# Kernel optimization log

Hardware: AMD Instinct MI355X
Metric: run time of the kernel (lower is better)

The kernel has to match this reference:

```python
import jax, jax.numpy as jnp
import numpy as np

B, T, S, H, C, E, V, OOV = 8, 16, 400, 512, 512, 128, 50000, 50


def setup_inputs() -> dict:
    key = jax.random.key(0)
    ks = jax.random.split(key, 24)
    rn = lambda k, shape, s=0.05: jax.random.normal(k, shape, dtype=jnp.float32) * s
    inp = {
        'input_embeddings': rn(ks[0], (B, T, E), 1.0),
        'context': rn(ks[1], (B, 1, C), 1.0),
        'h0': rn(ks[2], (1, B, H), 1.0),
        'c0': rn(ks[3], (1, B, H), 1.0),
        'encoder_outputs': rn(ks[4], (B, S, C), 1.0),
        'encoder_masks': jnp.ones((B, S), jnp.float32),
        'extra_zeros': jnp.zeros((B, OOV), jnp.float32),
        'extended_source_idx': jax.random.randint(ks[5], (B, S), 0, V + OOV),
        'coverage': jnp.zeros((B, 1, S), jnp.float32),
        # LSTM (single layer), torch gate order i,f,g,o
        'W_ih': rn(ks[6], (4 * H, E)), 'W_hh': rn(ks[7], (4 * H, H)),
        'b_ih': rn(ks[8], (4 * H,)), 'b_hh': rn(ks[9], (4 * H,)),
        # attention (concat + coverage)
        'cov_w': rn(ks[10], (H, 1)),
        'energy_w': rn(ks[11], (H, H + C)), 'energy_b': rn(ks[12], (H,)),
        'v': jax.random.uniform(ks[13], (H,), jnp.float32),
        # projections
        'xctx_w': rn(ks[14], (E, E + C)), 'xctx_b': rn(ks[15], (E,)),
        'attnd_w': rn(ks[16], (H, H + C)), 'attnd_b': rn(ks[17], (H,)),
        'vocab_w': rn(ks[18], (V, H)), 'vocab_b': rn(ks[19], (V,)),
        'pgen_w': rn(ks[20], (1, C + H + E)), 'pgen_b': rn(ks[21], (1,)),
    }
    return inp


def reference(input_embeddings, context, h0, c0, encoder_outputs, encoder_masks,
              extra_zeros, extended_source_idx, coverage,
              W_ih, W_hh, b_ih, b_hh, cov_w, energy_w, energy_b, v,
              xctx_w, xctx_b, attnd_w, attnd_b, vocab_w, vocab_b, pgen_w, pgen_b):
    Bn = input_embeddings.shape[0]
    Sn = encoder_outputs.shape[1]
    bidx = jnp.arange(Bn)[:, None]

    def step(carry, emb_t):
        h, c, ctx, cov = carry  # [B,H],[B,H],[B,C],[B,S]
        x = jnp.concatenate([emb_t, ctx], -1) @ xctx_w.T + xctx_b  # [B,E]
        gates = x @ W_ih.T + b_ih + h @ W_hh.T + b_hh
        i, f, g, o = jnp.split(gates, 4, axis=-1)
        c_new = jax.nn.sigmoid(f) * c + jax.nn.sigmoid(i) * jnp.tanh(g)
        h_new = jax.nn.sigmoid(o) * jnp.tanh(c_new)  # [B,H]
        # concat-style Luong attention with coverage
        cov_proj = cov[..., None] * cov_w[:, 0]  # [B,S,H] (Linear(1,H) no bias)
        cat = jnp.concatenate([
            jnp.broadcast_to(h_new[:, None, :], (Bn, Sn, h_new.shape[-1])),
            encoder_outputs], -1)  # [B,S,H+C]
        energy = jnp.tanh(cat @ energy_w.T + energy_b + cov_proj)
        e = energy @ v  # [B,S]
        probs = jax.nn.softmax(e, -1) * encoder_masks
        probs = probs / (probs.sum(-1, keepdims=True) + 1e-12)
        ctx_new = jnp.einsum('bs,bsc->bc', probs, encoder_outputs)
        cov_new = cov + probs
        vocab_dist = jax.nn.softmax(
            (jnp.concatenate([h_new, ctx_new], -1) @ attnd_w.T + attnd_b) @ vocab_w.T + vocab_b, -1)
        p_gen = jax.nn.sigmoid(jnp.concatenate([ctx_new, h_new, x], -1) @ pgen_w.T + pgen_b)  # [B,1]
        ext = jnp.concatenate([vocab_dist * p_gen, extra_zeros], 1)  # [B,V+OOV]
        final = ext.at[bidx, extended_source_idx].add((1.0 - p_gen) * probs)
        return (h_new, c_new, ctx_new, cov_new), (final, probs, cov_new, p_gen)

    init = (h0[0], c0[0], context[:, 0], coverage[:, 0])
    (h, c, ctx, cov), (finals, attns, covs, pgens) = jax.lax.scan(
        step, init, jnp.swapaxes(input_embeddings, 0, 1))
    final_vocab_dists = jnp.swapaxes(finals, 0, 1)  # [B,T,V+OOV]
    attn_dists = jnp.swapaxes(attns, 0, 1)          # [B,T,S]
    coverages = jnp.swapaxes(covs, 0, 1)            # [B,T,S]
    return (final_vocab_dists, ctx[:, None, :], h[None], c[None], attn_dists, pgens[-1], coverages)
```

## Files before the change

kernel.cpp:

```cpp
#include <hip/hip_runtime.h>
#include <math.h>

#define BB 8
#define TT 16
#define SS 400
#define HH 512
#define EE 128
#define VV 50000
#define VE 50050
#define OOVn 50

#define O1 6406400
#define O2 6410496
#define O3 6414592
#define O4 6418688
#define O5 6469888
#define O6 6469896

#define G_OFF    0
#define EWHB_OFF 1179648
#define AWBF_OFF 1310720
#define ENCP_OFF 4600000
#define PM_OFF   5700000
#define CTXR_OFF 5800000

typedef __attribute__((ext_vector_type(4))) float floatx4;
typedef __attribute__((ext_vector_type(8))) short short8;
typedef __attribute__((ext_vector_type(8))) unsigned short ushort8_t;
typedef __attribute__((ext_vector_type(4))) unsigned short ushort4_t;

__device__ __forceinline__ float sigm(float x){ return 1.0f/(1.0f+__expf(-x)); }
__device__ __forceinline__ float ftanh(float x){
  float e = __expf(2.0f*x); return 1.0f - 2.0f/(e + 1.0f);
}
__device__ __forceinline__ unsigned short f2bf(float f){
  union { float f; unsigned int u; } v; v.f = f;
  unsigned int u = v.u;
  return (unsigned short)((u + 0x7FFFu + ((u >> 16) & 1u)) >> 16);
}
__device__ __forceinline__ float bfu(unsigned short u){
  union { unsigned int i; float f; } v; v.i = ((unsigned int)u) << 16; return v.f;
}
__device__ __forceinline__ float mac8(const unsigned short* w, const float* u) {
  ushort8_t w8 = *(const ushort8_t*)w;
  float4 u0 = *(const float4*)u;
  float4 u1 = *(const float4*)(u+4);
  return bfu(w8[0])*u0.x + bfu(w8[1])*u0.y + bfu(w8[2])*u0.z + bfu(w8[3])*u0.w
       + bfu(w8[4])*u1.x + bfu(w8[5])*u1.y + bfu(w8[6])*u1.z + bfu(w8[7])*u1.w;
}

__global__ __launch_bounds__(256)
void gemm_bt(const float* __restrict__ A, int lda,
             const float* __restrict__ Bm, int ldb,
             const float* __restrict__ bias,
             float* __restrict__ Cm, int ldc,
             int N, int K, int permute, int obf,
             long bsB, long bsC)
{
  __shared__ unsigned short Ash[128*72];
  __shared__ unsigned short Bsh[64*72];
  int tid = threadIdx.x;
  int mbase = blockIdx.x * 128;
  int nbase = blockIdx.y * 64;
  long z = blockIdx.z;
  const float* Bz = Bm + z*bsB;
  int wave = tid >> 6, lane = tid & 63;
  int wm = (wave & 1) * 64, wn = (wave >> 1) * 32;
  int fl = lane & 15, quad = lane >> 4;

  floatx4 acc[4][2];
  for (int i=0;i<4;i++) for(int j=0;j<2;j++) acc[i][j] = (floatx4)(0.0f);

  for (int kc = 0; kc < K; kc += 64) {
    float4 ra[8], rb[4];
#pragma unroll
    for (int i = 0; i < 8; ++i) {
      int idx = tid + i*256;
      int row = idx >> 4;
      int c4 = (idx & 15) << 2;
      ra[i] = *(const float4*)(A + (size_t)(mbase+row)*lda + kc + c4);
    }
#pragma unroll
    for (int i = 0; i < 4; ++i) {
      int idx = tid + i*256;
      int row = idx >> 4;
      int c4 = (idx & 15) << 2;
      int gn = nbase + row;
      if (gn < N) rb[i] = *(const float4*)(Bz + (size_t)gn*ldb + kc + c4);
      else { rb[i].x = 0.f; rb[i].y = 0.f; rb[i].z = 0.f; rb[i].w = 0.f; }
    }
    __syncthreads();
#pragma unroll
    for (int i = 0; i < 8; ++i) {
      int idx = tid + i*256;
      int o = (idx >> 4)*72 + ((idx & 15) << 2);
      Ash[o+0]=f2bf(ra[i].x); Ash[o+1]=f2bf(ra[i].y); Ash[o+2]=f2bf(ra[i].z); Ash[o+3]=f2bf(ra[i].w);
    }
#pragma unroll
    for (int i = 0; i < 4; ++i) {
      int idx = tid + i*256;
      int o = (idx >> 4)*72 + ((idx & 15) << 2);
      Bsh[o+0]=f2bf(rb[i].x); Bsh[o+1]=f2bf(rb[i].y); Bsh[o+2]=f2bf(rb[i].z); Bsh[o+3]=f2bf(rb[i].w);
    }
    __syncthreads();
#pragma unroll
    for (int ks = 0; ks < 2; ++ks) {
      short8 af[4], bfr[2];
      int ko = ks*32 + quad*8;
#pragma unroll
      for (int i=0;i<4;i++) af[i]  = *(const short8*)&Ash[(wm + i*16 + fl)*72 + ko];
#pragma unroll
      for (int j=0;j<2;j++) bfr[j] = *(const short8*)&Bsh[(wn + j*16 + fl)*72 + ko];
#pragma unroll
      for (int i=0;i<4;i++)
#pragma unroll
        for (int j=0;j<2;j++)
          acc[i][j] = __builtin_amdgcn_mfma_f32_16x16x32_bf16(af[i], bfr[j], acc[i][j], 0,0,0);
    }
    __syncthreads();
  }
  for (int i=0;i<4;i++){
    for (int j=0;j<2;j++){
      int nc = nbase + wn + j*16 + fl;
      if (nc >= N) continue;
      float bv = bias ? bias[nc] : 0.0f;
      for (int r=0;r<4;r++){
        int mg = mbase + wm + i*16 + quad*4 + r;
        int orow = permute ? ((mg & 7)*16 + (mg >> 3)) : mg;
        float v = acc[i][j][r] + bv;
        long ci = (long)orow*ldc + nc + z*bsC;
        if (obf) ((unsigned short*)Cm)[ci] = f2bf(v);
        else     Cm[ci] = v;
      }
    }
  }
}

__global__ __launch_bounds__(256)
void gemm_logits(const unsigned short* __restrict__ Abf,
                 const float* __restrict__ Bm, const float* __restrict__ bias,
                 float* __restrict__ out, float* __restrict__ rowsum)
{
  __shared__ unsigned short Ash[128*72];
  __shared__ unsigned short Bsh[64*72];
  __shared__ float rowpart[128];
  int tid = threadIdx.x;
  int nbase = blockIdx.x * 64;
  int wave = tid >> 6, lane = tid & 63;
  int wm = (wave & 1) * 64, wn = (wave >> 1) * 32;
  int fl = lane & 15, quad = lane >> 4;

  floatx4 acc[4][2];
  for (int i=0;i<4;i++) for(int j=0;j<2;j++) acc[i][j] = (floatx4)(0.0f);
  if (tid < 128) rowpart[tid] = 0.f;

  for (int kc = 0; kc < 512; kc += 64) {
    ushort8_t raa[4];
    float4 rb[4];
#pragma unroll
    for (int i = 0; i < 4; ++i) {
      int idx = tid + i*256;
      int row = idx >> 3;
      int c8 = (idx & 7) << 3;
      raa[i] = *(const ushort8_t*)(Abf + (size_t)row*512 + kc + c8);
    }
#pragma unroll
    for (int i = 0; i < 4; ++i) {
      int idx = tid + i*256;
      int row = idx >> 4;
      int c4 = (idx & 15) << 2;
      int gn = nbase + row;
      if (gn < VV) rb[i] = *(const float4*)(Bm + (size_t)gn*512 + kc + c4);
      else { rb[i].x = 0.f; rb[i].y = 0.f; rb[i].z = 0.f; rb[i].w = 0.f; }
    }
    __syncthreads();
#pragma unroll
    for (int i = 0; i < 4; ++i) {
      int idx = tid + i*256;
      int o = (idx >> 3)*72 + ((idx & 7) << 3);
      *(ushort8_t*)&Ash[o] = raa[i];
    }
#pragma unroll
    for (int i = 0; i < 4; ++i) {
      int idx = tid + i*256;
      int o = (idx >> 4)*72 + ((idx & 15) << 2);
      Bsh[o+0]=f2bf(rb[i].x); Bsh[o+1]=f2bf(rb[i].y); Bsh[o+2]=f2bf(rb[i].z); Bsh[o+3]=f2bf(rb[i].w);
    }
    __syncthreads();
#pragma unroll
    for (int ks = 0; ks < 2; ++ks) {
      short8 af[4], bfr[2];
      int ko = ks*32 + quad*8;
#pragma unroll
      for (int i=0;i<4;i++) af[i]  = *(const short8*)&Ash[(wm + i*16 + fl)*72 + ko];
#pragma unroll
      for (int j=0;j<2;j++) bfr[j] = *(const short8*)&Bsh[(wn + j*16 + fl)*72 + ko];
#pragma unroll
      for (int i=0;i<4;i++)
#pragma unroll
        for (int j=0;j<2;j++)
          acc[i][j] = __builtin_amdgcn_mfma_f32_16x16x32_bf16(af[i], bfr[j], acc[i][j], 0,0,0);
    }
    __syncthreads();
  }
  for (int i=0;i<4;i++){
    for (int r=0;r<4;r++){
      int mg = wm + i*16 + quad*4 + r;
      int orow = (mg & 7)*16 + (mg >> 3);
      float rs = 0.f;
      for (int j=0;j<2;j++){
        int nc = nbase + wn + j*16 + fl;
        if (nc < VV) {
          float e = __expf(acc[i][j][r] + bias[nc]);
          out[(size_t)orow*VE + nc] = e;
          rs += e;
        }
      }
      atomicAdd(&rowpart[mg], rs);
    }
  }
  __syncthreads();
  if (tid < 128) {
    int orow = (tid & 7)*16 + (tid >> 3);
    atomicAdd(&rowsum[orow], rowpart[tid]);
  }
}

__global__ __launch_bounds__(256) void vk_attnd(
    const float* __restrict__ A1, const unsigned short* __restrict__ awbf,
    const float* __restrict__ ab, unsigned short* __restrict__ attnd_bf)
{
  __shared__ float hl[8][1032];
  __shared__ float part[256];
  int tid = threadIdx.x;
  int pc = blockIdx.x & 63;
  int mg = blockIdx.x >> 6;
  int m0 = mg*8;
#pragma unroll
  for (int i = 0; i < 8; ++i)
    *(float4*)&hl[i][tid*4] = *(const float4*)(A1 + (size_t)(m0+i)*1024 + tid*4);
  __syncthreads();
  int dot = tid >> 2, kq = tid & 3;
  int lp = dot >> 3, lm = dot & 7;
  int p = pc*8 + lp;
  const unsigned short* wp = awbf + (size_t)p*1024 + kq*16;
  const float* hh = &hl[lm][kq*16];
  float acc = 0.f;
#pragma unroll
  for (int i = 0; i < 16; ++i) {
    acc += mac8(wp + i*64, hh + i*64);
    acc += mac8(wp + i*64 + 8, hh + i*64 + 8);
  }
  part[tid] = acc;
  __syncthreads();
  if (tid < 64) {
    int lp2 = tid >> 3, lm2 = tid & 7;
    int p2 = pc*8 + lp2;
    float v = ab[p2] + part[tid*4] + part[tid*4+1] + part[tid*4+2] + part[tid*4+3];
    attnd_bf[(size_t)(m0+lm2)*512 + p2] = f2bf(v);
  }
}

__global__ __launch_bounds__(256) void p_wx(const float* __restrict__ wih,
    const float* __restrict__ whh, const float* __restrict__ xcw,
    unsigned short* __restrict__ G)
{
  int blk = blockIdx.x, tid = threadIdx.x;
  if (blk < 640) {
    int rt = blk / 10, ct = blk % 10;
    __shared__ float wl[32*128];
    __shared__ float xl[128*64];
    for (int i = tid; i < 4096; i += 256) {
      int r = i >> 7, k = i & 127;
      wl[i] = wih[(size_t)(rt*32+r)*128 + k];
    }
    for (int i = tid; i < 8192; i += 256) {
      int e = i >> 6, c = i & 63;
      xl[i] = xcw[(size_t)e*640 + ct*64 + c];
    }
    __syncthreads();
    for (int o = tid; o < 2048; o += 256) {
      int r = o >> 6, c = o & 63;
      float acc = 0.f;
      for (int e = 0; e < 128; ++e) acc += wl[r*128+e]*xl[e*64+c];
      G[(size_t)(rt*32+r)*1152 + ct*64 + c] = f2bf(acc);
    }
  } else {
    int idx = blk - 640;
    for (int q = 0; q < 2; ++q) {
      int n = idx*2048 + q*1024 + tid*4;
      int r = n >> 9, k = n & 511;
      float4 v = *(const float4*)(whh + n);
      ushort4_t s; s[0]=f2bf(v.x); s[1]=f2bf(v.y); s[2]=f2bf(v.z); s[3]=f2bf(v.w);
      *(ushort4_t*)(G + (size_t)r*1152 + 640 + k) = s;
    }
  }
}

__global__ __launch_bounds__(256) void p_small(const float* __restrict__ wih,
    const float* __restrict__ bih, const float* __restrict__ bhh,
    const float* __restrict__ xb, const float* __restrict__ xcw,
    const float* __restrict__ pw, const float* __restrict__ pb,
    float* __restrict__ gb, float* __restrict__ q, float* __restrict__ qb,
    float* __restrict__ d1, float* __restrict__ d2)
{
  int blk = blockIdx.x, tid = threadIdx.x;
  if (blk < 8) {
    __shared__ float xbl[128];
    if (tid < 128) xbl[tid] = xb[tid];
    __syncthreads();
    int r = blk*256 + tid;
    const float* wr = wih + (size_t)r*128;
    float acc = bih[r] + bhh[r];
    for (int e = 0; e < 128; ++e) acc += wr[e]*xbl[e];
    gb[r] = acc;
  } else if (blk < 11) {
    int o = (blk-8)*256 + tid;
    if (o < 640) {
      float acc = 0.f;
      for (int e = 0; e < 128; ++e) acc += pw[1024+e]*xcw[(size_t)e*640 + o];
      q[o] = acc;
    }
  } else {
    if (tid == 0) {
      float acc = 0.f;
      for (int e = 0; e < 128; ++e) acc += pw[1024+e]*xb[e];
      qb[0] = acc + pb[0];
    }
    if (tid < 128) { d1[tid] = 0.f; d2[tid] = 0.f; }
  }
}

__global__ __launch_bounds__(256) void p_cast(const float* __restrict__ ew,
    unsigned short* __restrict__ ewhb, const float* __restrict__ aw,
    unsigned short* __restrict__ awbf, float* __restrict__ ctxraw)
{
  int blk = blockIdx.x, tid = threadIdx.x;
  if (blk < 128) {
    for (int q = 0; q < 2; ++q) {
      size_t n = (size_t)blk*2048 + q*1024 + tid*4;
      int p = (int)(n >> 9), k = (int)(n & 511);
      float4 v = *(const float4*)(ew + (size_t)p*1024 + k);
      ushort4_t s; s[0]=f2bf(v.x); s[1]=f2bf(v.y); s[2]=f2bf(v.z); s[3]=f2bf(v.w);
      *(ushort4_t*)(ewhb + n) = s;
    }
    for (int i = tid; i < 512; i += 256) ctxraw[(size_t)blk*512 + i] = 0.f;
  } else {
    int idx = blk - 128;
    for (int q = 0; q < 4; ++q) {
      size_t n = (size_t)idx*4096 + q*1024 + tid*4;
      float4 v = *(const float4*)(aw + n);
      ushort4_t s; s[0]=f2bf(v.x); s[1]=f2bf(v.y); s[2]=f2bf(v.z); s[3]=f2bf(v.w);
      *(ushort4_t*)(awbf + n) = s;
    }
  }
}

__global__ __launch_bounds__(256) void s1g(
    const unsigned short* __restrict__ G,
    const float* __restrict__ gb,
    const float* __restrict__ emb, const float* __restrict__ context,
    const float* __restrict__ h0, const float* __restrict__ c0,
    const float* __restrict__ coverage,
    const float* __restrict__ PM, const float* __restrict__ d1,
    const float* __restrict__ d2, const float* __restrict__ ctxraw,
    float* __restrict__ A1, float* __restrict__ c_cur,
    float* __restrict__ out, int t)
{
  __shared__ float ueh[8][644];
  __shared__ float uc[8][516];
  __shared__ float part[256];
  __shared__ float gl[64];
  __shared__ float invs[8];
  int tid = threadIdx.x, blk = blockIdx.x;

  if (t >= 1 && tid < 8)
    invs[tid] = 1.0f / (d2[(t-1)*8 + tid] + 1e-12f*d1[(t-1)*8 + tid]);
  __syncthreads();

  for (int i = 0; i < 5; ++i) {
    int slot = i*256 + tid;
    int b = slot / 160, sl = slot - b*160;
    if (sl < 32) {
      *(float4*)&ueh[b][sl*4] = *(const float4*)(emb + (size_t)(b*16+t)*128 + sl*4);
    } else {
      int qq = sl - 32;
      const float* hsrc = t ? (A1 + ((size_t)((t-1)*8+b))*1024) : (h0 + b*512);
      *(float4*)&ueh[b][128 + qq*4] = *(const float4*)(hsrc + qq*4);
    }
  }
  for (int i = 0; i < 4; ++i) {
    int slot = i*256 + tid;
    int b = slot >> 7, sl = slot & 127;
    const float* csrc = t ? (ctxraw + ((size_t)((t-1)*8+b))*512)
                          : (context + (size_t)b*512);
    float4 v = *(const float4*)(csrc + sl*4);
    if (t) { float iv = invs[b]; v.x*=iv; v.y*=iv; v.z*=iv; v.w*=iv; }
    *(float4*)&uc[b][sl*4] = v;
  }
  __syncthreads();

  if (t >= 1 && blk < 8) {
    int b = blk;
    float iv = invs[b];
    const float* covprev = (t == 1) ? (coverage + b*400)
                                    : (out + O6 + ((size_t)(b*16 + t-2))*400);
    const float* pmsrc = PM + (size_t)(t-1)*3200 + b*400;
    size_t o = ((size_t)(b*16 + t-1))*400;
    for (int s = tid; s < 400; s += 256) {
      float pr = pmsrc[s] * iv;
      out[O4 + o + s] = pr;
      out[O6 + o + s] = covprev[s] + pr;
    }
  }

  int dot = tid >> 2, kq = tid & 3;
  int rr = dot >> 3, b = dot & 7;
  int gate = rr >> 1, jj = rr & 1;
  int r = gate*512 + blk*2 + jj;
  const unsigned short* gr = G + (size_t)r*1152;
  float acc = 0.f;
  {
    const unsigned short* gp = gr + kq*8;
    const float* up = &ueh[b][kq*8];
#pragma unroll
    for (int i = 0; i < 4; ++i) acc += mac8(gp + i*32, up + i*32);
  }
  {
    const unsigned short* gp = gr + 128 + kq*8;
    const float* up = &uc[b][kq*8];
#pragma unroll 4
    for (int i = 0; i < 16; ++i) acc += mac8(gp + i*32, up + i*32);
  }
  {
    const unsigned short* gp = gr + 640 + kq*8;
    const float* up = &ueh[b][128 + kq*8];
#pragma unroll 4
    for (int i = 0; i < 16; ++i) acc += mac8(gp + i*32, up + i*32);
  }
  part[tid] = acc;
  __syncthreads();
  if (tid < 64) {
    int rr2 = tid >> 3;
    int r2 = (rr2 >> 1)*512 + blk*2 + (rr2 & 1);
    gl[tid] = part[tid*4] + part[tid*4+1] + part[tid*4+2] + part[tid*4+3] + gb[r2];
  }
  __syncthreads();
  if (tid < 16) {
    int jj2 = tid >> 3, b2 = tid & 7;
    float gi = gl[(0*2+jj2)*8 + b2];
    float gf = gl[(1*2+jj2)*8 + b2];
    float gg = gl[(2*2+jj2)*8 + b2];
    float go = gl[(3*2+jj2)*8 + b2];
    int j = blk*2 + jj2;
    float cp = t ? c_cur[b2*512+j] : c0[b2*512+j];
    float cn = sigm(gf)*cp + sigm(gi)*ftanh(gg);
    float hn = sigm(go)*ftanh(cn);
    c_cur[b2*512+j] = cn;
    A1[((size_t)(t*8+b2))*1024 + j] = hn;
  }
}

__global__ __launch_bounds__(256) void s2_hp(
    const unsigned short* __restrict__ ewhb, const float* __restrict__ eb,
    const float* __restrict__ A1, float* __restrict__ hp, int t)
{
  __shared__ float hl[8*516];
  __shared__ float part[256];
  int tid = threadIdx.x, pc = blockIdx.x;
  for (int b = 0; b < 8; ++b)
    for (int k = tid; k < 512; k += 256)
      hl[b*516 + k] = A1[((size_t)(t*8+b))*1024 + k];
  __syncthreads();
  int dot = tid >> 2, kq = tid & 3;
  int rr = dot >> 3, b = dot & 7;
  int p = pc*8 + rr;
  const unsigned short* wp = ewhb + (size_t)p*512 + kq*16;
  const float* hh = hl + b*516 + kq*16;
  float acc = 0.f;
#pragma unroll
  for (int i = 0; i < 8; ++i) {
    acc += mac8(wp + i*64, hh + i*64);
    acc += mac8(wp + i*64 + 8, hh + i*64 + 8);
  }
  part[tid] = acc;
  __syncthreads();
  if (tid < 64) {
    int rr2 = tid >> 3, b2 = tid & 7;
    int p2 = pc*8 + rr2;
    hp[b2*512 + p2] = eb[p2] + part[tid*4] + part[tid*4+1] + part[tid*4+2] + part[tid*4+3];
  }
}

__global__ __launch_bounds__(256) void s3e(
    const unsigned short* __restrict__ encpb, const float* __restrict__ hp,
    const float* __restrict__ vvec, const float* __restrict__ covw,
    const float* __restrict__ masks, const float* __restrict__ coverage,
    const float* __restrict__ out6v, const float* __restrict__ enc,
    float* __restrict__ PM, float* __restrict__ d1, float* __restrict__ d2,
    float* __restrict__ ctxraw, int t)
{
  int tid = threadIdx.x;
  int b = blockIdx.x >> 4, sc = blockIdx.x & 15;
  int w = tid >> 6, lane = tid & 63;
  int h0i = lane*8;
  __shared__ float red1[4], red2[4];
  __shared__ float pms[25];
  float hpv[8], vv[8], cw[8];
  {
    const float* hpp = hp + b*512 + h0i;
    float4 a0 = *(const float4*)(hpp), a1 = *(const float4*)(hpp+4);
    hpv[0]=a0.x; hpv[1]=a0.y; hpv[2]=a0.z; hpv[3]=a0.w;
    hpv[4]=a1.x; hpv[5]=a1.y; hpv[6]=a1.z; hpv[7]=a1.w;
    float4 v0 = *(const float4*)(vvec+h0i), v1 = *(const float4*)(vvec+h0i+4);
    vv[0]=v0.x; vv[1]=v0.y; vv[2]=v0.z; vv[3]=v0.w;
    vv[4]=v1.x; vv[5]=v1.y; vv[6]=v1.z; vv[7]=v1.w;
    float4 c0v = *(const float4*)(covw+h0i), c1v = *(const float4*)(covw+h0i+4);
    cw[0]=c0v.x; cw[1]=c0v.y; cw[2]=c0v.z; cw[3]=c0v.w;
    cw[4]=c1v.x; cw[5]=c1v.y; cw[6]=c1v.z; cw[7]=c1v.w;
  }
  const float* covp = t ? (out6v + ((size_t)(b*16 + t-1))*400) : (coverage + b*400);
  float a1s = 0.f, a2s = 0.f;
  for (int sl = w; sl < 25; sl += 4) {
    int s = sc*25 + sl;
    float cv = covp[s];
    const unsigned short* ep = encpb + ((size_t)(b*400+s))*512 + h0i;
    ushort8_t e8 = *(const ushort8_t*)ep;
    float acc = 0.f;
#pragma unroll
    for (int i = 0; i < 8; ++i)
      acc += ftanh(hpv[i] + bfu(e8[i]) + cv*cw[i]) * vv[i];
    for (int off = 32; off > 0; off >>= 1) acc += __shfl_down(acc, off);
    if (lane == 0) {
      float pe = __expf(acc);
      float pmv = pe * masks[b*400 + s];
      PM[(size_t)t*3200 + b*400 + s] = pmv;
      pms[sl] = pmv;
      a1s += pe; a2s += pmv;
    }
  }
  if (lane == 0) { red1[w] = a1s; red2[w] = a2s; }
  __syncthreads();
  if (tid == 0) {
    atomicAdd(&d1[t*8+b], red1[0]+red1[1]+red1[2]+red1[3]);
    atomicAdd(&d2[t*8+b], red2[0]+red2[1]+red2[2]+red2[3]);
  }
  {
    float acc0 = 0.f, acc1 = 0.f;
    const float* encb = enc + ((size_t)(b*400 + sc*25))*512;
#pragma unroll 5
    for (int sl = 0; sl < 25; ++sl) {
      float pmv = pms[sl];
      const float* er = encb + (size_t)sl*512;
      acc0 += pmv * er[tid];
      acc1 += pmv * er[tid + 256];
    }
    float* cr = ctxraw + ((size_t)(t*8+b))*512;
    atomicAdd(&cr[tid], acc0);
    atomicAdd(&cr[tid+256], acc1);
  }
}

__global__ __launch_bounds__(256) void e_pgen(
    const float* __restrict__ A1f, const float* __restrict__ c_cur,
    const float* __restrict__ emb, const float* __restrict__ context,
    const float* __restrict__ pw, const float* __restrict__ q,
    const float* __restrict__ qb,
    const float* __restrict__ d1, const float* __restrict__ d2,
    const float* __restrict__ ctxraw, const float* __restrict__ PM,
    float* __restrict__ A1, float* __restrict__ pgen,
    float* __restrict__ rowsum, float* __restrict__ out)
{
  int blk = blockIdx.x, tid = threadIdx.x;
  if (blk < 128) {
    int m = blk, t = m >> 3, b = m & 7;
    __shared__ float invT, invP;
    if (tid == 0) invT = 1.0f / (d2[m] + 1e-12f*d1[m]);
    if (tid == 64) invP = t ? 1.0f / (d2[m-8] + 1e-12f*d1[m-8]) : 0.f;
    __syncthreads();
    const float* crT = ctxraw + (size_t)m*512;
    const float* crP = ctxraw + (size_t)(t ? m-8 : m)*512;
    const float* hT   = A1f + (size_t)m*1024;
    const float* embp = emb + (size_t)(b*16+t)*128;
    float acc = 0.f;
    for (int k = tid; k < 512; k += 256) {
      float cT = crT[k] * invT;
      float cP = t ? crP[k] * invP : context[(size_t)b*512 + k];
      acc += pw[k]*cT + pw[512+k]*hT[k] + q[128+k]*cP;
      A1[(size_t)m*1024 + 512 + k] = cT;
    }
    if (tid < 128) acc += q[tid]*embp[tid];
    for (int off = 32; off > 0; off >>= 1) acc += __shfl_down(acc, off);
    __shared__ float red[4];
    if (!(tid & 63)) red[tid>>6] = acc;
    __syncthreads();
    if (tid == 0) {
      float pg = sigm(red[0]+red[1]+red[2]+red[3] + qb[0]);
      pgen[m] = pg;
      if (t == 15) out[O5 + b] = pg;
    }
  } else if (blk == 128) {
    for (int i = tid; i < 4096; i += 256) {
      int b = i >> 9, j = i & 511;
      float inv = 1.0f / (d2[120+b] + 1e-12f*d1[120+b]);
      out[O1 + i] = ctxraw[(size_t)(120+b)*512 + j] * inv;
    }
  } else if (blk == 129) {
    for (int i = tid; i < 4096; i += 256) {
      int b = i >> 9, j = i & 511;
      out[O2 + i] = A1f[((size_t)(120+b))*1024 + j];
    }
  } else if (blk == 130) {
    for (int i = tid; i < 4096; i += 256) out[O3 + i] = c_cur[i];
  } else if (blk == 131) {
    if (tid < 128) rowsum[tid] = 0.f;
  } else {
    int b = blk - 132;
    float inv = 1.0f / (d2[120+b] + 1e-12f*d1[120+b]);
    const float* pmsrc = PM + (size_t)15*3200 + b*400;
    size_t o15 = ((size_t)(b*16 + 15))*400;
    size_t o14 = ((size_t)(b*16 + 14))*400;
    for (int s = tid; s < 400; s += 256) {
      float pr = pmsrc[s] * inv;
      out[O4 + o15 + s] = pr;
      out[O6 + o15 + s] = out[O6 + o14 + s] + pr;
    }
  }
}

__global__ __launch_bounds__(256) void k_scale(
    float* __restrict__ out, const float* __restrict__ pgen,
    const float* __restrict__ rowsum, const float* __restrict__ ez,
    const int* __restrict__ extidx)
{
  int orow = blockIdx.x, cy = blockIdx.y, tid = threadIdx.x;
  int b = orow >> 4, t = orow & 15;
  float sc = pgen[t*8+b] / rowsum[orow];
  int c0 = cy*6256;
  int c1 = (cy == 7) ? VE : c0 + 6256;
  float* row = out + (size_t)orow*VE;
  for (int c = c0 + tid*4; c < c1; c += 1024) {
    if (c + 4 <= VV && c + 4 <= c1) {
      float4 v = *(float4*)(row + c);
      v.x *= sc; v.y *= sc; v.z *= sc; v.w *= sc;
      *(float4*)(row + c) = v;
    } else {
      for (int e = 0; e < 4; ++e) {
        int cc2 = c + e;
        if (cc2 < c1) row[cc2] = (cc2 < VV) ? row[cc2]*sc : ez[b*OOVn + cc2 - VV];
      }
    }
  }
  __syncthreads();
  float onem = 1.0f - pgen[t*8+b];
  const float* pr = out + O4 + (size_t)orow*SS;
  for (int s = tid; s < SS; s += 256) {
    int ix = extidx[b*SS + s];
    if (ix >= c0 && ix < c1)
      atomicAdd(&row[ix], onem * pr[s]);
  }
}

extern "C" void kernel_launch(void* const* d_in, const int* in_sizes, int n_in,
                              void* d_out, int out_size, void* d_ws, size_t ws_size,
                              hipStream_t stream)
{
  (void)in_sizes; (void)n_in; (void)out_size; (void)ws_size;
  const float* emb      = (const float*)d_in[0];
  const float* context  = (const float*)d_in[1];
  const float* h0       = (const float*)d_in[2];
  const float* c0       = (const float*)d_in[3];
  const float* enc      = (const float*)d_in[4];
  const float* masks    = (const float*)d_in[5];
  const float* ez       = (const float*)d_in[6];
  const int*   extidx   = (const int*)d_in[7];
  const float* coverage = (const float*)d_in[8];
  const float* wih      = (const float*)d_in[9];
  const float* whh      = (const float*)d_in[10];
  const float* bih      = (const float*)d_in[11];
  const float* bhh      = (const float*)d_in[12];
  const float* covw     = (const float*)d_in[13];
  const float* ew       = (const float*)d_in[14];
  const float* eb       = (const float*)d_in[15];
  const float* vvec     = (const float*)d_in[16];
  const float* xw       = (const float*)d_in[17];
  const float* xb       = (const float*)d_in[18];
  const float* aw       = (const float*)d_in[19];
  const float* ab       = (const float*)d_in[20];
  const float* vw       = (const float*)d_in[21];
  const float* vb       = (const float*)d_in[22];
  const float* pw       = (const float*)d_in[23];
  const float* pb       = (const float*)d_in[24];
  float* out = (float*)d_out;

  float* ws = (float*)d_ws;
  float* A1       = ws;
  float* c_cur    = ws + 131072;
  float* hp       = ws + 135168;
  unsigned short* attnd_bf = (unsigned short*)(ws + 139264);
  float* pgen     = ws + 172032;
  float* gb       = ws + 172160;
  float* q        = ws + 174208;
  float* qb       = ws + 174848;
  float* d1       = ws + 174852;
  float* d2       = ws + 174980;
  float* rowsum   = ws + 175108;

  unsigned short* G     = (unsigned short*)(out + G_OFF);
  unsigned short* ewhb  = (unsigned short*)(out + EWHB_OFF);
  unsigned short* awbf  = (unsigned short*)(out + AWBF_OFF);
  unsigned short* encpb = (unsigned short*)(out + ENCP_OFF);
  float*          PM    = out + PM_OFF;
  float*          ctxr  = out + CTXR_OFF;

  p_wx<<<1152, 256, 0, stream>>>(wih, whh, xw, G);
  p_small<<<12, 256, 0, stream>>>(wih, bih, bhh, xb, xw, pw, pb, gb, q, qb, d1, d2);
  p_cast<<<256, 256, 0, stream>>>(ew, ewhb, aw, awbf, ctxr);
  gemm_bt<<<dim3(25,8,1), 256, 0, stream>>>(enc, 512, ew + 512, 1024,
      (const float*)nullptr, (float*)encpb, 512, 512, 512, 0, 1, 0, 0);

  for (int t = 0; t < TT; ++t) {
    s1g<<<256, 256, 0, stream>>>(G, gb, emb, context, h0, c0, coverage,
                                 PM, d1, d2, ctxr, A1, c_cur, out, t);
    s2_hp<<<64, 256, 0, stream>>>(ewhb, eb, A1, hp, t);
    s3e<<<128, 256, 0, stream>>>(encpb, hp, vvec, covw, masks, coverage,
                                 out + O6, enc, PM, d1, d2, ctxr, t);
  }

  e_pgen<<<140, 256, 0, stream>>>(A1, c_cur, emb, context, pw, q, qb,
                                  d1, d2, ctxr, PM, A1, pgen, rowsum, out);
  vk_attnd<<<1024, 256, 0, stream>>>(A1, awbf, ab, attnd_bf);
  gemm_logits<<<782, 256, 0, stream>>>(attnd_bf, vw, vb, out, rowsum);
  k_scale<<<dim3(128,8), 256, 0, stream>>>(out, pgen, rowsum, ez, extidx);
}
```

Baseline: 746.2 us.

## Fuse per-step LSTM, projection and attention kernels with atomic-counter inter-block sync

Merges the three per-timestep kernels into one 448-block launch. Block roles are split by index, and roles are ordered with global atomic counters and spin-waits instead of kernel boundaries. Attention blocks prefetch their encoder-projection tiles and masks into shared memory before waiting, so those loads overlap the LSTM and projection phases. This removes two launches per step, but correctness depends on all 448 blocks being co-resident to avoid deadlock, and the spinning may cost cycles.

Measured after the change: 1.375 ms. 84.3% more time.

```diff
diff --git a/kernel.cpp b/kernel.cpp
--- a/kernel.cpp
+++ b/kernel.cpp
@@ -302,7 +302,8 @@
     const float* __restrict__ xb, const float* __restrict__ xcw,
     const float* __restrict__ pw, const float* __restrict__ pb,
     float* __restrict__ gb, float* __restrict__ q, float* __restrict__ qb,
-    float* __restrict__ d1, float* __restrict__ d2)
+    float* __restrict__ d1, float* __restrict__ d2,
+    unsigned int* __restrict__ ctr)
 {
   int blk = blockIdx.x, tid = threadIdx.x;
   if (blk < 8) {
@@ -328,6 +329,7 @@
       qb[0] = acc + pb[0];
     }
     if (tid < 128) { d1[tid] = 0.f; d2[tid] = 0.f; }
+    if (tid < 32) ctr[tid] = 0u;
   }
 }
 
@@ -356,208 +358,231 @@
   }
 }
 
-__global__ __launch_bounds__(256) void s1g(
+__global__ __launch_bounds__(256) void step_f(
     const unsigned short* __restrict__ G,
+    const unsigned short* __restrict__ encpb,
+    const unsigned short* __restrict__ ewhb,
     const float* __restrict__ gb,
     const float* __restrict__ emb, const float* __restrict__ context,
     const float* __restrict__ h0, const float* __restrict__ c0,
-    const float* __restrict__ coverage,
-    const float* __restrict__ PM, const float* __restrict__ d1,
-    const float* __restrict__ d2, const float* __restrict__ ctxraw,
-    float* __restrict__ A1, float* __restrict__ c_cur,
-    float* __restrict__ out, int t)
-{
-  __shared__ float ueh[8][644];
-  __shared__ float uc[8][516];
-  __shared__ float part[256];
-  __shared__ float gl[64];
-  __shared__ float invs[8];
+    const float* __restrict__ coverage, const float* __restrict__ masks,
+    const float* __restrict__ enc, const float* __restrict__ vvec,
+    const float* __restrict__ covw, const float* __restrict__ eb,
+    float* __restrict__ PM, float* __restrict__ d1, float* __restrict__ d2,
+    float* __restrict__ ctxraw, float* __restrict__ A1,
+    float* __restrict__ c_cur, float* __restrict__ hp,
+    float* __restrict__ out,
+    unsigned int* __restrict__ ctrA, unsigned int* __restrict__ ctrB, int t)
+{
+  union ShU {
+    struct { float ueh[8][644]; float uc[8][516]; float part[256];
+             float gl[64]; float invs[8]; } a;
+    struct { float hl[8*516]; float part[256]; } b;
+    struct { unsigned short eps[25][512]; float pms[25];
+             float red1[4]; float red2[4]; float msk[25]; } c;
+  };
+  __shared__ ShU sh;
   int tid = threadIdx.x, blk = blockIdx.x;
 
-  if (t >= 1 && tid < 8)
-    invs[tid] = 1.0f / (d2[(t-1)*8 + tid] + 1e-12f*d1[(t-1)*8 + tid]);
-  __syncthreads();
-
-  for (int i = 0; i < 5; ++i) {
-    int slot = i*256 + tid;
-    int b = slot / 160, sl = slot - b*160;
-    if (sl < 32) {
-      *(float4*)&ueh[b][sl*4] = *(const float4*)(emb + (size_t)(b*16+t)*128 + sl*4);
-    } else {
-      int qq = sl - 32;
-      const float* hsrc = t ? (A1 + ((size_t)((t-1)*8+b))*1024) : (h0 + b*512);
-      *(float4*)&ueh[b][128 + qq*4] = *(const float4*)(hsrc + qq*4);
-    }
-  }
-  for (int i = 0; i < 4; ++i) {
-    int slot = i*256 + tid;
-    int b = slot >> 7, sl = slot & 127;
-    const float* csrc = t ? (ctxraw + ((size_t)((t-1)*8+b))*512)
-                          : (context + (size_t)b*512);
-    float4 v = *(const float4*)(csrc + sl*4);
-    if (t) { float iv = invs[b]; v.x*=iv; v.y*=iv; v.z*=iv; v.w*=iv; }
-    *(float4*)&uc[b][sl*4] = v;
-  }
-  __syncthreads();
-
-  if (t >= 1 && blk < 8) {
-    int b = blk;
-    float iv = invs[b];
-    const float* covprev = (t == 1) ? (coverage + b*400)
-                                    : (out + O6 + ((size_t)(b*16 + t-2))*400);
-    const float* pmsrc = PM + (size_t)(t-1)*3200 + b*400;
-    size_t o = ((size_t)(b*16 + t-1))*400;
-    for (int s = tid; s < 400; s += 256) {
-      float pr = pmsrc[s] * iv;
-      out[O4 + o + s] = pr;
-      out[O6 + o + s] = covprev[s] + pr;
-    }
-  }
-
-  int dot = tid >> 2, kq = tid & 3;
-  int rr = dot >> 3, b = dot & 7;
-  int gate = rr >> 1, jj = rr & 1;
-  int r = gate*512 + blk*2 + jj;
-  const unsigned short* gr = G + (size_t)r*1152;
-  float acc = 0.f;
-  {
-    const unsigned short* gp = gr + kq*8;
-    const float* up = &ueh[b][kq*8];
-#pragma unroll
-    for (int i = 0; i < 4; ++i) acc += mac8(gp + i*32, up + i*32);
-  }
-  {
-    const unsigned short* gp = gr + 128 + kq*8;
-    const float* up = &uc[b][kq*8];
+  if (blk < 256) {
+    if (t >= 1 && tid < 8)
+      sh.a.invs[tid] = 1.0f / (d2[(t-1)*8 + tid] + 1e-12f*d1[(t-1)*8 + tid]);
+    __syncthreads();
+
+    for (int i = 0; i < 5; ++i) {
+      int slot = i*256 + tid;
+      int b = slot / 160, sl = slot - b*160;
+      if (sl < 32) {
+        *(float4*)&sh.a.ueh[b][sl*4] = *(const float4*)(emb + (size_t)(b*16+t)*128 + sl*4);
+      } else {
+        int qq = sl - 32;
+        const float* hsrc = t ? (A1 + ((size_t)((t-1)*8+b))*1024) : (h0 + b*512);
+        *(float4*)&sh.a.ueh[b][128 + qq*4] = *(const float4*)(hsrc + qq*4);
+      }
+    }
+    for (int i = 0; i < 4; ++i) {
+      int slot = i*256 + tid;
+      int b = slot >> 7, sl = slot & 127;
+      const float* csrc = t ? (ctxraw + ((size_t)((t-1)*8+b))*512)
+                            : (context + (size_t)b*512);
+      float4 v = *(const float4*)(csrc + sl*4);
+      if (t) { float iv = sh.a.invs[b]; v.x*=iv; v.y*=iv; v.z*=iv; v.w*=iv; }
+      *(float4*)&sh.a.uc[b][sl*4] = v;
+    }
+    __syncthreads();
+
+    if (t >= 1 && blk < 8) {
+      int b = blk;
+      float iv = sh.a.invs[b];
+      const float* covprev = (t == 1) ? (coverage + b*400)
+                                      : (out + O6 + ((size_t)(b*16 + t-2))*400);
+      const float* pmsrc = PM + (size_t)(t-1)*3200 + b*400;
+      size_t o = ((size_t)(b*16 + t-1))*400;
+      for (int s = tid; s < 400; s += 256) {
+        float pr = pmsrc[s] * iv;
+        out[O4 + o + s] = pr;
+        out[O6 + o + s] = covprev[s] + pr;
+      }
+    }
+
+    {
+      int dot = tid >> 2, kq = tid & 3;
+      int rr = dot >> 3, b = dot & 7;
+      int gate = rr >> 1, jj = rr & 1;
+      int r = gate*512 + blk*2 + jj;
+      const unsigned short* gr = G + (size_t)r*1152;
+      float acc = 0.f;
+      {
+        const unsigned short* gp = gr + kq*8;
+        const float* up = &sh.a.ueh[b][kq*8];
+#pragma unroll
+        for (int i = 0; i < 4; ++i) acc += mac8(gp + i*32, up + i*32);
+      }
+      {
+        const unsigned short* gp = gr + 128 + kq*8;
+        const float* up = &sh.a.uc[b][kq*8];
 #pragma unroll 4
-    for (int i = 0; i < 16; ++i) acc += mac8(gp + i*32, up + i*32);
-  }
-  {
-    const unsigned short* gp = gr + 640 + kq*8;
-    const float* up = &ueh[b][128 + kq*8];
+        for (int i = 0; i < 16; ++i) acc += mac8(gp + i*32, up + i*32);
+      }
+      {
+        const unsigned short* gp = gr + 640 + kq*8;
+        const float* up = &sh.a.ueh[b][128 + kq*8];
 #pragma unroll 4
-    for (int i = 0; i < 16; ++i) acc += mac8(gp + i*32, up + i*32);
-  }
-  part[tid] = acc;
-  __syncthreads();
-  if (tid < 64) {
-    int rr2 = tid >> 3;
-    int r2 = (rr2 >> 1)*512 + blk*2 + (rr2 & 1);
-    gl[tid] = part[tid*4] + part[tid*4+1] + part[tid*4+2] + part[tid*4+3] + gb[r2];
-  }
-  __syncthreads();
-  if (tid < 16) {
-    int jj2 = tid >> 3, b2 = tid & 7;
-    float gi = gl[(0*2+jj2)*8 + b2];
-    float gf = gl[(1*2+jj2)*8 + b2];
-    float gg = gl[(2*2+jj2)*8 + b2];
-    float go = gl[(3*2+jj2)*8 + b2];
-    int j = blk*2 + jj2;
-    float cp = t ? c_cur[b2*512+j] : c0[b2*512+j];
-    float cn = sigm(gf)*cp + sigm(gi)*ftanh(gg);
-    float hn = sigm(go)*ftanh(cn);
-    c_cur[b2*512+j] = cn;
-    A1[((size_t)(t*8+b2))*1024 + j] = hn;
-  }
-}
-
-__global__ __launch_bounds__(256) void s2_hp(
-    const unsigned short* __restrict__ ewhb, const float* __restrict__ eb,
-    const float* __restrict__ A1, float* __restrict__ hp, int t)
-{
-  __shared__ float hl[8*516];
-  __shared__ float part[256];
-  int tid = threadIdx.x, pc = blockIdx.x;
-  for (int b = 0; b < 8; ++b)
-    for (int k = tid; k < 512; k += 256)
-      hl[b*516 + k] = A1[((size_t)(t*8+b))*1024 + k];
-  __syncthreads();
-  int dot = tid >> 2, kq = tid & 3;
-  int rr = dot >> 3, b = dot & 7;
-  int p = pc*8 + rr;
-  const unsigned short* wp = ewhb + (size_t)p*512 + kq*16;
-  const float* hh = hl + b*516 + kq*16;
-  float acc = 0.f;
-#pragma unroll
-  for (int i = 0; i < 8; ++i) {
-    acc += mac8(wp + i*64, hh + i*64);
-    acc += mac8(wp + i*64 + 8, hh + i*64 + 8);
-  }
-  part[tid] = acc;
-  __syncthreads();
-  if (tid < 64) {
-    int rr2 = tid >> 3, b2 = tid & 7;
-    int p2 = pc*8 + rr2;
-    hp[b2*512 + p2] = eb[p2] + part[tid*4] + part[tid*4+1] + part[tid*4+2] + part[tid*4+3];
-  }
-}
-
-__global__ __launch_bounds__(256) void s3e(
-    const unsigned short* __restrict__ encpb, const float* __restrict__ hp,
-    const float* __restrict__ vvec, const float* __restrict__ covw,
-    const float* __restrict__ masks, const float* __restrict__ coverage,
-    const float* __restrict__ out6v, const float* __restrict__ enc,
-    float* __restrict__ PM, float* __restrict__ d1, float* __restrict__ d2,
-    float* __restrict__ ctxraw, int t)
-{
-  int tid = threadIdx.x;
-  int b = blockIdx.x >> 4, sc = blockIdx.x & 15;
-  int w = tid >> 6, lane = tid & 63;
-  int h0i = lane*8;
-  __shared__ float red1[4], red2[4];
-  __shared__ float pms[25];
-  float hpv[8], vv[8], cw[8];
-  {
-    const float* hpp = hp + b*512 + h0i;
-    float4 a0 = *(const float4*)(hpp), a1 = *(const float4*)(hpp+4);
-    hpv[0]=a0.x; hpv[1]=a0.y; hpv[2]=a0.z; hpv[3]=a0.w;
-    hpv[4]=a1.x; hpv[5]=a1.y; hpv[6]=a1.z; hpv[7]=a1.w;
-    float4 v0 = *(const float4*)(vvec+h0i), v1 = *(const float4*)(vvec+h0i+4);
-    vv[0]=v0.x; vv[1]=v0.y; vv[2]=v0.z; vv[3]=v0.w;
-    vv[4]=v1.x; vv[5]=v1.y; vv[6]=v1.z; vv[7]=v1.w;
-    float4 c0v = *(const float4*)(covw+h0i), c1v = *(const float4*)(covw+h0i+4);
-    cw[0]=c0v.x; cw[1]=c0v.y; cw[2]=c0v.z; cw[3]=c0v.w;
-    cw[4]=c1v.x; cw[5]=c1v.y; cw[6]=c1v.z; cw[7]=c1v.w;
-  }
-  const float* covp = t ? (out6v + ((size_t)(b*16 + t-1))*400) : (coverage + b*400);
-  float a1s = 0.f, a2s = 0.f;
-  for (int sl = w; sl < 25; sl += 4) {
-    int s = sc*25 + sl;
-    float cv = covp[s];
-    const unsigned short* ep = encpb + ((size_t)(b*400+s))*512 + h0i;
-    ushort8_t e8 = *(const ushort8_t*)ep;
+        for (int i = 0; i < 16; ++i) acc += mac8(gp + i*32, up + i*32);
+      }
+      sh.a.part[tid] = acc;
+    }
+    __syncthreads();
+    if (tid < 64) {
+      int rr2 = tid >> 3;
+      int r2 = (rr2 >> 1)*512 + blk*2 + (rr2 & 1);
+      sh.a.gl[tid] = sh.a.part[tid*4] + sh.a.part[tid*4+1]
+                   + sh.a.part[tid*4+2] + sh.a.part[tid*4+3] + gb[r2];
+    }
+    __syncthreads();
+    if (tid < 16) {
+      int jj2 = tid >> 3, b2 = tid & 7;
+      float gi = sh.a.gl[(0*2+jj2)*8 + b2];
+      float gf = sh.a.gl[(1*2+jj2)*8 + b2];
+      float gg = sh.a.gl[(2*2+jj2)*8 + b2];
+      float go = sh.a.gl[(3*2+jj2)*8 + b2];
+      int j = blk*2 + jj2;
+      float cp = t ? c_cur[b2*512+j] : c0[b2*512+j];
+      float cn = sigm(gf)*cp + sigm(gi)*ftanh(gg);
+      float hn = sigm(go)*ftanh(cn);
+      c_cur[b2*512+j] = cn;
+      A1[((size_t)(t*8+b2))*1024 + j] = hn;
+    }
+    __syncthreads();
+    __threadfence();
+    if (tid == 0) atomicAdd(ctrA, 1u);
+
+  } else if (blk < 320) {
+    int pc = blk - 256;
+    if (tid == 0) {
+      while (atomicAdd(ctrA, 0u) < 256u) __builtin_amdgcn_s_sleep(8);
+    }
+    __syncthreads();
+    __threadfence();
+    for (int b = 0; b < 8; ++b)
+      for (int k = tid; k < 512; k += 256)
+        sh.b.hl[b*516 + k] = A1[((size_t)(t*8+b))*1024 + k];
+    __syncthreads();
+    int dot = tid >> 2, kq = tid & 3;
+    int rr = dot >> 3, b = dot & 7;
+    int p = pc*8 + rr;
+    const unsigned short* wp = ewhb + (size_t)p*512 + kq*16;
+    const float* hh = sh.b.hl + b*516 + kq*16;
     float acc = 0.f;
 #pragma unroll
-    for (int i = 0; i < 8; ++i)
-      acc += ftanh(hpv[i] + bfu(e8[i]) + cv*cw[i]) * vv[i];
-    for (int off = 32; off > 0; off >>= 1) acc += __shfl_down(acc, off);
-    if (lane == 0) {
-      float pe = __expf(acc);
-      float pmv = pe * masks[b*400 + s];
-      PM[(size_t)t*3200 + b*400 + s] = pmv;
-      pms[sl] = pmv;
-      a1s += pe; a2s += pmv;
-    }
-  }
-  if (lane == 0) { red1[w] = a1s; red2[w] = a2s; }
-  __syncthreads();
-  if (tid == 0) {
-    atomicAdd(&d1[t*8+b], red1[0]+red1[1]+red1[2]+red1[3]);
-    atomicAdd(&d2[t*8+b], red2[0]+red2[1]+red2[2]+red2[3]);
-  }
-  {
-    float acc0 = 0.f, acc1 = 0.f;
-    const float* encb = enc + ((size_t)(b*400 + sc*25))*512;
+    for (int i = 0; i < 8; ++i) {
+      acc += mac8(wp + i*64, hh + i*64);
+      acc += mac8(wp + i*64 + 8, hh + i*64 + 8);
+    }
+    sh.b.part[tid] = acc;
+    __syncthreads();
+    if (tid < 64) {
+      int rr2 = tid >> 3, b2 = tid & 7;
+      int p2 = pc*8 + rr2;
+      hp[b2*512 + p2] = eb[p2] + sh.b.part[tid*4] + sh.b.part[tid*4+1]
+                      + sh.b.part[tid*4+2] + sh.b.part[tid*4+3];
+    }
+    __syncthreads();
+    __threadfence();
+    if (tid == 0) atomicAdd(ctrB, 1u);
+
+  } else {
+    int bb = (blk - 320) >> 4, sc = (blk - 320) & 15;
+    int w = tid >> 6, lane = tid & 63;
+    int h0i = lane*8;
+    for (int i = tid; i < 1600; i += 256) {
+      int sl = i >> 6, seg = i & 63;
+      *(ushort8_t*)&sh.c.eps[sl][seg*8] =
+          *(const ushort8_t*)(encpb + ((size_t)(bb*400 + sc*25 + sl))*512 + seg*8);
+    }
+    if (tid < 25) sh.c.msk[tid] = masks[bb*400 + sc*25 + tid];
+    float vv[8], cw[8];
+    {
+      float4 v0 = *(const float4*)(vvec+h0i), v1 = *(const float4*)(vvec+h0i+4);
+      vv[0]=v0.x; vv[1]=v0.y; vv[2]=v0.z; vv[3]=v0.w;
+      vv[4]=v1.x; vv[5]=v1.y; vv[6]=v1.z; vv[7]=v1.w;
+      float4 c0v = *(const float4*)(covw+h0i), c1v = *(const float4*)(covw+h0i+4);
+      cw[0]=c0v.x; cw[1]=c0v.y; cw[2]=c0v.z; cw[3]=c0v.w;
+      cw[4]=c1v.x; cw[5]=c1v.y; cw[6]=c1v.z; cw[7]=c1v.w;
+    }
+    if (tid == 0) {
+      while (atomicAdd(ctrA, 0u) < 256u || atomicAdd(ctrB, 0u) < 64u)
+        __builtin_amdgcn_s_sleep(8);
+    }
+    __syncthreads();
+    __threadfence();
+    float hpv[8];
+    {
+      const float* hpp = hp + bb*512 + h0i;
+      float4 q0 = *(const float4*)(hpp), q1 = *(const float4*)(hpp+4);
+      hpv[0]=q0.x; hpv[1]=q0.y; hpv[2]=q0.z; hpv[3]=q0.w;
+      hpv[4]=q1.x; hpv[5]=q1.y; hpv[6]=q1.z; hpv[7]=q1.w;
+    }
+    const float* covp = t ? (out + O6 + ((size_t)(bb*16 + t-1))*400)
+                          : (coverage + bb*400);
+    float a1s = 0.f, a2s = 0.f;
+    for (int sl = w; sl < 25; sl += 4) {
+      int s = sc*25 + sl;
+      float cv = covp[s];
+      ushort8_t e8 = *(const ushort8_t*)&sh.c.eps[sl][h0i];
+      float acc = 0.f;
+#pragma unroll
+      for (int i = 0; i < 8; ++i)
+        acc += ftanh(hpv[i] + bfu(e8[i]) + cv*cw[i]) * vv[i];
+      for (int off = 32; off > 0; off >>= 1) acc += __shfl_down(acc, off);
+      if (lane == 0) {
+        float pe = __expf(acc);
+        float pmv = pe * sh.c.msk[sl];
+        PM[(size_t)t*3200 + bb*400 + s] = pmv;
+        sh.c.pms[sl] = pmv;
+        a1s += pe; a2s += pmv;
+      }
+    }
+    if (lane == 0) { sh.c.red1[w] = a1s; sh.c.red2[w] = a2s; }
+    __syncthreads();
+    if (tid == 0) {
+      atomicAdd(&d1[t*8+bb], sh.c.red1[0]+sh.c.red1[1]+sh.c.red1[2]+sh.c.red1[3]);
+      atomicAdd(&d2[t*8+bb], sh.c.red2[0]+sh.c.red2[1]+sh.c.red2[2]+sh.c.red2[3]);
+    }
+    {
+      float acc0 = 0.f, acc1 = 0.f;
+      const float* encb = enc + ((size_t)(bb*400 + sc*25))*512;
 #pragma unroll 5
-    for (int sl = 0; sl < 25; ++sl) {
-      float pmv = pms[sl];
-      const float* er = encb + (size_t)sl*512;
-      acc0 += pmv * er[tid];
-      acc1 += pmv * er[tid + 256];
-    }
-    float* cr = ctxraw + ((size_t)(t*8+b))*512;
-    atomicAdd(&cr[tid], acc0);
-    atomicAdd(&cr[tid+256], acc1);
+      for (int sl = 0; sl < 25; ++sl) {
+        float pmv = sh.c.pms[sl];
+        const float* er = encb + (size_t)sl*512;
+        acc0 += pmv * er[tid];
+        acc1 += pmv * er[tid + 256];
+      }
+      float* cr = ctxraw + ((size_t)(t*8+bb))*512;
+      atomicAdd(&cr[tid], acc0);
+      atomicAdd(&cr[tid+256], acc1);
+    }
   }
 }
 
@@ -705,6 +730,7 @@
   float* d1       = ws + 174852;
   float* d2       = ws + 174980;
   float* rowsum   = ws + 175108;
+  unsigned int* ctr = (unsigned int*)(ws + 175236);
 
   unsigned short* G     = (unsigned short*)(out + G_OFF);
   unsigned short* ewhb  = (unsigned short*)(out + EWHB_OFF);
@@ -714,17 +740,17 @@
   float*          ctxr  = out + CTXR_OFF;
 
   p_wx<<<1152, 256, 0, stream>>>(wih, whh, xw, G);
-  p_small<<<12, 256, 0, stream>>>(wih, bih, bhh, xb, xw, pw, pb, gb, q, qb, d1, d2);
+  p_small<<<12, 256, 0, stream>>>(wih, bih, bhh, xb, xw, pw, pb, gb, q, qb,
+                                  d1, d2, ctr);
   p_cast<<<256, 256, 0, stream>>>(ew, ewhb, aw, awbf, ctxr);
   gemm_bt<<<dim3(25,8,1), 256, 0, stream>>>(enc, 512, ew + 512, 1024,
       (const float*)nullptr, (float*)encpb, 512, 512, 512, 0, 1, 0, 0);
 
   for (int t = 0; t < TT; ++t) {
-    s1g<<<256, 256, 0, stream>>>(G, gb, emb, context, h0, c0, coverage,
-                                 PM, d1, d2, ctxr, A1, c_cur, out, t);
-    s2_hp<<<64, 256, 0, stream>>>(ewhb, eb, A1, hp, t);
-    s3e<<<128, 256, 0, stream>>>(encpb, hp, vvec, covw, masks, coverage,
-                                 out + O6, enc, PM, d1, d2, ctxr, t);
+    step_f<<<448, 256, 0, stream>>>(G, encpb, ewhb, gb, emb, context, h0, c0,
+                                    coverage, masks, enc, vvec, covw, eb,
+                                    PM, d1, d2, ctxr, A1, c_cur, hp, out,
+                                    ctr + 2*t, ctr + 2*t + 1, t);
   }
 
   e_pgen<<<140, 256, 0, stream>>>(A1, c_cur, emb, context, pw, q, qb,
```
